# Kernel tuning notes

Measured on AMD Instinct MI355X. Metric: run time of the kernel, lower is better.

## Reference

```python
import jax, jax.numpy as jnp
import numpy as np

N_QUBITS = 16
N_LAYERS = 2
BATCH = 32


def _rx(theta):
    # RX(t) = [[cos(t/2), -i sin(t/2)], [-i sin(t/2), cos(t/2)]]
    # theta: scalar -> (2,2); (B,) -> (B,2,2)
    c = jnp.cos(theta / 2).astype(jnp.complex64)
    s = (-1j * jnp.sin(theta / 2)).astype(jnp.complex64)
    return jnp.stack([jnp.stack([c, s], -1), jnp.stack([s, c], -1)], -2)


def _apply_1q(state, U, wire):
    # state: (B, 2, ..., 2); U: (2,2) shared or (B,2,2) per-sample
    s = jnp.moveaxis(state, wire + 1, 1)
    if U.ndim == 3:
        s = jnp.einsum('bij,bj...->bi...', U, s)
    else:
        s = jnp.einsum('ij,bj...->bi...', U, s)
    return jnp.moveaxis(s, 1, wire + 1)


def _apply_cnot(state, ctrl, tgt):
    # flip target axis where control axis == 1
    s = jnp.moveaxis(state, (ctrl + 1, tgt + 1), (1, 2))
    s = s.at[:, 1].set(s[:, 1, ::-1])
    return jnp.moveaxis(s, (1, 2), (ctrl + 1, tgt + 1))


def _circuit(x, weights):
    n = N_QUBITS
    B = x.shape[0]
    state = jnp.zeros((B, 2 ** n), dtype=jnp.complex64)
    state = state.at[:, 0].set(1.0)
    state = state.reshape((B,) + (2,) * n)
    # AngleEmbedding: RX(x[:, w]) on each wire (per-sample angles)
    for w in range(n):
        state = _apply_1q(state, _rx(x[:, w]), w)
    # BasicEntanglerLayers: per layer, RX(weights[l, w]) then ring of CNOTs
    for l in range(N_LAYERS):
        for w in range(n):
            state = _apply_1q(state, _rx(weights[l, w]), w)
        for w in range(n):
            state = _apply_cnot(state, w, (w + 1) % n)
    # <Z_w> = sum_s |amp_s|^2 * (1 - 2*bit_w(s))
    p = jnp.abs(state.reshape(B, 2 ** n)) ** 2  # (B, 2^n) float32
    idx = jnp.arange(2 ** n)
    bits = (idx[:, None] >> (n - 1 - jnp.arange(n)[None, :])) & 1  # axis order = wire order (MSB first)
    signs = (1 - 2 * bits).astype(jnp.float32)  # (2^n, n)
    return p @ signs  # (B, n)


def setup_inputs() -> dict:
    key = jax.random.key(0)
    k1, k2 = jax.random.split(key)
    x = jax.random.normal(k1, (BATCH, N_QUBITS), dtype=jnp.float32)
    weights = jax.random.uniform(k2, (N_LAYERS, N_QUBITS), dtype=jnp.float32,
                                 minval=0.0, maxval=2.0 * np.pi)
    return {"x": x, "weights": weights}


def reference(x, weights):
    return _circuit(x, weights)
```

## Files before the change

### kernel.cpp

```cpp
#include <hip/hip_runtime.h>
#include <math.h>


#define NQ 16
#define BATCH 32

struct Cpx { float re, im; };
__device__ __forceinline__ Cpx cmul(Cpx a, Cpx b) {
    return { a.re * b.re - a.im * b.im, a.re * b.im + a.im * b.re };
}
__device__ __forceinline__ Cpx cadd(Cpx a, Cpx b) {
    return { a.re + b.re, a.im + b.im };
}

__global__ __launch_bounds__(64) void qnn_transfer_kernel(
        const float* __restrict__ x,
        const float* __restrict__ wt,
        float* __restrict__ out)
{
    const int t = blockIdx.x * 64 + threadIdx.x;
    if (t >= BATCH * NQ) return;
    const int b = t >> 4;
    const int w = t & 15;

    float pc[NQ], ps[NQ], kc[NQ], ks[NQ];
    #pragma unroll
    for (int q = 0; q < NQ; ++q) {
        float t1 = x[b * NQ + q] + wt[q];
        float th = wt[NQ + q];
        sincosf(0.5f * t1, &ps[q], &pc[q]);
        sincosf(th,        &ks[q], &kc[q]);
    }

    Cpx V[4][4];
    #pragma unroll
    for (int i = 0; i < 4; ++i) {
        const int al  = i & 1;
        const int alp = (i >> 1) & 1;
        Cpx fk = al  ? Cpx{0.f, -ps[0]} : Cpx{pc[0], 0.f};
        Cpx fb = alp ? Cpx{0.f,  ps[0]} : Cpx{pc[0], 0.f};
        Cpx f = cmul(fk, fb);
        #pragma unroll
        for (int j = 0; j < 4; ++j) V[i][j] = (j == i) ? f : Cpx{0.f, 0.f};
    }

    #pragma unroll
    for (int q = 1; q < NQ; ++q) {
        const bool inQ = (w == 0) ? true : (q <= w);
        const Cpx f0 = { pc[q], 0.f }, f1 = { 0.f, -ps[q] };
        const Cpx g0 = { pc[q], 0.f }, g1 = { 0.f,  ps[q] };
        Cpx M00, M01, M10, M11;
        if (inQ) { M00 = {kc[q], 0.f}; M01 = {0.f, -ks[q]};
                   M10 = {0.f, ks[q]}; M11 = {-kc[q], 0.f}; }
        else     { M00 = {1.f, 0.f};   M01 = {0.f, 0.f};
                   M10 = {0.f, 0.f};   M11 = {1.f, 0.f}; }
        #pragma unroll
        for (int i = 0; i < 4; ++i) {
            Cpx v00 = V[i][0], v01 = V[i][1], v10 = V[i][2], v11 = V[i][3];
            Cpx u00 = cadd(cmul(f0, v00), cmul(f1, v01));
            Cpx u01 = cadd(cmul(f1, v00), cmul(f0, v01));
            Cpx u10 = cadd(cmul(f0, v10), cmul(f1, v11));
            Cpx u11 = cadd(cmul(f1, v10), cmul(f0, v11));
            Cpx z00 = cadd(cmul(g0, u00), cmul(g1, u10));
            Cpx z01 = cadd(cmul(g0, u01), cmul(g1, u11));
            Cpx z10 = cadd(cmul(g1, u00), cmul(g0, u10));
            Cpx z11 = cadd(cmul(g1, u01), cmul(g0, u11));
            V[i][0] = cmul(M00, z00);
            V[i][1] = cmul(M01, z01);
            V[i][2] = cmul(M10, z10);
            V[i][3] = cmul(M11, z11);
        }
    }

    const bool q0in = (w >= 1);
    Cpx N00, N01, N10, N11;
    if (q0in) { N00 = {kc[0], 0.f}; N01 = {0.f, -ks[0]};
                N10 = {0.f, ks[0]}; N11 = {-kc[0], 0.f}; }
    else      { N00 = {1.f, 0.f};   N01 = {0.f, 0.f};
                N10 = {0.f, 0.f};   N11 = {1.f, 0.f}; }

    float acc = 0.f;
    #pragma unroll
    for (int i = 0; i < 4; ++i) {
        const int al  = i & 1;
        const int alp = (i >> 1) & 1;
        #pragma unroll
        for (int j = 0; j < 4; ++j) {
            const int be  = j & 1;
            const int bep = (j >> 1) & 1;
            const int row = bep ^ alp;
            const int col = be ^ al;
            Cpx m = (row == 0) ? (col == 0 ? N00 : N01)
                               : (col == 0 ? N10 : N11);
            acc += cmul(m, V[i][j]).re;
        }
    }
    out[b * NQ + w] = acc;
}

extern "C" void kernel_launch(void* const* d_in, const int* in_sizes, int n_in,
                              void* d_out, int out_size, void* d_ws, size_t ws_size,
                              hipStream_t stream) {
    const float* x  = (const float*)d_in[0];
    const float* wt = (const float*)d_in[1];
    float* out = (float*)d_out;
    (void)in_sizes; (void)n_in; (void)out_size; (void)d_ws; (void)ws_size;

    qnn_transfer_kernel<<<(BATCH * NQ + 63) / 64, 64, 0, stream>>>(x, wt, out);
}
```

Measured before the change: 68.04 us.

## Split transfer-matrix rows across lanes and share trig values via LDS

Launches one block per batch sample and gives each of four lanes one row of the 4x4 transfer matrix instead of one thread doing all rows. The sincos values are computed once per block by 16 threads and kept in shared memory rather than redundantly in every thread. The complex arithmetic is hand-expanded to real ops that exploit the purely real or imaginary gate entries. The four partial sums are combined with xor shuffles. This cuts per-thread serial work and register pressure at the cost of a barrier and cross-lane reduction; total runtime is likely dominated by launch overhead anyway.

```diff
diff --git a/kernel.cpp b/kernel.cpp
--- a/kernel.cpp
+++ b/kernel.cpp
@@ -5,97 +5,74 @@
 #define NQ 16
 #define BATCH 32
 
-struct Cpx { float re, im; };
-__device__ __forceinline__ Cpx cmul(Cpx a, Cpx b) {
-    return { a.re * b.re - a.im * b.im, a.re * b.im + a.im * b.re };
-}
-__device__ __forceinline__ Cpx cadd(Cpx a, Cpx b) {
-    return { a.re + b.re, a.im + b.im };
-}
-
 __global__ __launch_bounds__(64) void qnn_transfer_kernel(
         const float* __restrict__ x,
         const float* __restrict__ wt,
         float* __restrict__ out)
 {
-    const int t = blockIdx.x * 64 + threadIdx.x;
-    if (t >= BATCH * NQ) return;
-    const int b = t >> 4;
-    const int w = t & 15;
+    const int b   = blockIdx.x;
+    const int tid = threadIdx.x;
+    const int w   = tid >> 2;
+    const int br  = tid & 3;
+    const int al  = br & 1;
+    const int alp = (br >> 1) & 1;
 
-    float pc[NQ], ps[NQ], kc[NQ], ks[NQ];
-    #pragma unroll
-    for (int q = 0; q < NQ; ++q) {
-        float t1 = x[b * NQ + q] + wt[q];
-        float th = wt[NQ + q];
-        sincosf(0.5f * t1, &ps[q], &pc[q]);
-        sincosf(th,        &ks[q], &kc[q]);
+    __shared__ float pc[NQ], ps[NQ], kc[NQ], ks[NQ];
+    if (tid < NQ) {
+        float t1 = x[b * NQ + tid] + wt[tid];
+        float th = wt[NQ + tid];
+        float sp, cp, sk, ck;
+        sincosf(0.5f * t1, &sp, &cp);
+        sincosf(th,        &sk, &ck);
+        pc[tid] = cp; ps[tid] = sp; kc[tid] = ck; ks[tid] = sk;
     }
+    __syncthreads();
 
-    Cpx V[4][4];
-    #pragma unroll
-    for (int i = 0; i < 4; ++i) {
-        const int al  = i & 1;
-        const int alp = (i >> 1) & 1;
-        Cpx fk = al  ? Cpx{0.f, -ps[0]} : Cpx{pc[0], 0.f};
-        Cpx fb = alp ? Cpx{0.f,  ps[0]} : Cpx{pc[0], 0.f};
-        Cpx f = cmul(fk, fb);
-        #pragma unroll
-        for (int j = 0; j < 4; ++j) V[i][j] = (j == i) ? f : Cpx{0.f, 0.f};
-    }
+    const float c0 = pc[0], s0 = ps[0];
+    float v00r = (br == 0) ? c0 * c0 : 0.f, v00i = 0.f;
+    float v01r = 0.f, v01i = (br == 1) ? -s0 * c0 : 0.f;
+    float v10r = 0.f, v10i = (br == 2) ?  s0 * c0 : 0.f;
+    float v11r = (br == 3) ? s0 * s0 : 0.f, v11i = 0.f;
 
     #pragma unroll
     for (int q = 1; q < NQ; ++q) {
+        const float c = pc[q], s = ps[q];
         const bool inQ = (w == 0) ? true : (q <= w);
-        const Cpx f0 = { pc[q], 0.f }, f1 = { 0.f, -ps[q] };
-        const Cpx g0 = { pc[q], 0.f }, g1 = { 0.f,  ps[q] };
-        Cpx M00, M01, M10, M11;
-        if (inQ) { M00 = {kc[q], 0.f}; M01 = {0.f, -ks[q]};
-                   M10 = {0.f, ks[q]}; M11 = {-kc[q], 0.f}; }
-        else     { M00 = {1.f, 0.f};   M01 = {0.f, 0.f};
-                   M10 = {0.f, 0.f};   M11 = {1.f, 0.f}; }
-        #pragma unroll
-        for (int i = 0; i < 4; ++i) {
-            Cpx v00 = V[i][0], v01 = V[i][1], v10 = V[i][2], v11 = V[i][3];
-            Cpx u00 = cadd(cmul(f0, v00), cmul(f1, v01));
-            Cpx u01 = cadd(cmul(f1, v00), cmul(f0, v01));
-            Cpx u10 = cadd(cmul(f0, v10), cmul(f1, v11));
-            Cpx u11 = cadd(cmul(f1, v10), cmul(f0, v11));
-            Cpx z00 = cadd(cmul(g0, u00), cmul(g1, u10));
-            Cpx z01 = cadd(cmul(g0, u01), cmul(g1, u11));
-            Cpx z10 = cadd(cmul(g1, u00), cmul(g0, u10));
-            Cpx z11 = cadd(cmul(g1, u01), cmul(g0, u11));
-            V[i][0] = cmul(M00, z00);
-            V[i][1] = cmul(M01, z01);
-            V[i][2] = cmul(M10, z10);
-            V[i][3] = cmul(M11, z11);
-        }
+        const float a = inQ ?  kc[q] : 1.f;
+        const float e = inQ ?  ks[q] : 0.f;
+        const float d = inQ ? -kc[q] : 1.f;
+
+        float u00r =  c * v00r + s * v01i, u00i =  c * v00i - s * v01r;
+        float u01r =  s * v00i + c * v01r, u01i = -s * v00r + c * v01i;
+        float u10r =  c * v10r + s * v11i, u10i =  c * v10i - s * v11r;
+        float u11r =  s * v10i + c * v11r, u11i = -s * v10r + c * v11i;
+        float z00r =  c * u00r - s * u10i, z00i =  c * u00i + s * u10r;
+        float z01r =  c * u01r - s * u11i, z01i =  c * u01i + s * u11r;
+        float z10r = -s * u00i + c * u10r, z10i =  s * u00r + c * u10i;
+        float z11r = -s * u01i + c * u11r, z11i =  s * u01r + c * u11i;
+        v00r =  a * z00r;  v00i =  a * z00i;
+        v01r =  e * z01i;  v01i = -e * z01r;
+        v10r = -e * z10i;  v10i =  e * z10r;
+        v11r =  d * z11r;  v11i =  d * z11i;
     }
 
     const bool q0in = (w >= 1);
-    Cpx N00, N01, N10, N11;
-    if (q0in) { N00 = {kc[0], 0.f}; N01 = {0.f, -ks[0]};
-                N10 = {0.f, ks[0]}; N11 = {-kc[0], 0.f}; }
-    else      { N00 = {1.f, 0.f};   N01 = {0.f, 0.f};
-                N10 = {0.f, 0.f};   N11 = {1.f, 0.f}; }
+    const float A = q0in ?  kc[0] : 1.f;
+    const float B = q0in ?  ks[0] : 0.f;
+    const float D = q0in ? -kc[0] : 1.f;
 
-    float acc = 0.f;
-    #pragma unroll
-    for (int i = 0; i < 4; ++i) {
-        const int al  = i & 1;
-        const int alp = (i >> 1) & 1;
-        #pragma unroll
-        for (int j = 0; j < 4; ++j) {
-            const int be  = j & 1;
-            const int bep = (j >> 1) & 1;
-            const int row = bep ^ alp;
-            const int col = be ^ al;
-            Cpx m = (row == 0) ? (col == 0 ? N00 : N01)
-                               : (col == 0 ? N10 : N11);
-            acc += cmul(m, V[i][j]).re;
-        }
-    }
-    out[b * NQ + w] = acc;
+    auto contrib = [&](int row, int col, float Vr, float Vi) -> float {
+        return row ? (col ? D * Vr : -B * Vi)
+                   : (col ? B * Vi :  A * Vr);
+    };
+    float acc = contrib(alp,     al,     v00r, v00i)
+              + contrib(alp,     al ^ 1, v01r, v01i)
+              + contrib(alp ^ 1, al,     v10r, v10i)
+              + contrib(alp ^ 1, al ^ 1, v11r, v11i);
+
+    acc += __shfl_xor(acc, 1);
+    acc += __shfl_xor(acc, 2);
+    if (br == 0) out[b * NQ + w] = acc;
 }
 
 extern "C" void kernel_launch(void* const* d_in, const int* in_sizes, int n_in,
@@ -106,5 +83,5 @@
     float* out = (float*)d_out;
     (void)in_sizes; (void)n_in; (void)out_size; (void)d_ws; (void)ws_size;
 
-    qnn_transfer_kernel<<<(BATCH * NQ + 63) / 64, 64, 0, stream>>>(x, wt, out);
+    qnn_transfer_kernel<<<BATCH, 64, 0, stream>>>(x, wt, out);
 }
```

New measurement: 55.29 us. 18.7% less time.
